# Kernel optimization log

Hardware: AMD Instinct MI355X
Metric: run time of the kernel (lower is better)

## Reference

```python
import jax, jax.numpy as jnp
import numpy as np

H = 8          # n_heads
THRESH = 0.5   # edge pruning threshold
LN_EPS = 1e-5


def setup_inputs() -> dict:
    key = jax.random.key(0)
    ks = jax.random.split(key, 24)
    B, S, D = 8, 128, 256
    N = S + 1
    hd = D // H

    def lin(k, fan_in, fan_out, gain=1.0):
        # xavier_uniform-ish init, stored as [in, out] (y = x @ W + b)
        lim = gain * np.sqrt(6.0 / (fan_in + fan_out))
        return jax.random.uniform(k, (fan_in, fan_out), jnp.float32, -lim, lim)

    g = 1.0 / np.sqrt(2.0)
    return {
        "desc": jax.random.normal(ks[0], (B, S, D), jnp.float32),
        "nv": jax.random.normal(ks[1], (B, N, D), jnp.float32),
        "W_gt": lin(ks[2], D, D), "b_gt": jnp.zeros((D,), jnp.float32),
        "topo_bias": jnp.zeros((1,), jnp.float32),
        "W_q": lin(ks[3], D, D, g), "b_q": jnp.zeros((D,), jnp.float32),
        "W_k": lin(ks[4], D, D, g), "b_k": jnp.zeros((D,), jnp.float32),
        "W_v": lin(ks[5], D, D, g), "b_v": jnp.zeros((D,), jnp.float32),
        "W_e1": lin(ks[6], 2 * D, D), "b_e1": jnp.zeros((D,), jnp.float32),
        "ln_g": jnp.ones((D,), jnp.float32), "ln_b": jnp.zeros((D,), jnp.float32),
        "W_e2": lin(ks[7], D, D), "b_e2": jnp.zeros((D,), jnp.float32),
        "w_attn": lin(ks[8], 3 * hd, 1, g)[:, 0], "b_attn": jnp.zeros((), jnp.float32),
        "W_o": lin(ks[9], D, D, g), "b_o": jnp.zeros((D,), jnp.float32),
    }


def _forward(desc, nv, W_gt, b_gt, topo_bias, W_q, b_q, W_k, b_k, W_v, b_v,
             W_e1, b_e1, ln_g, ln_b, W_e2, b_e2, w_attn, b_attn, W_o, b_o):
    B, N, D = nv.shape
    S = N - 1
    hd = D // H

    # 1. global topology
    d = desc @ W_gt + b_gt                                   # [B,S,D]
    dn = d / jnp.linalg.norm(d, axis=-1, keepdims=True)
    global_top = jax.nn.sigmoid(jnp.einsum('bid,bjd->bij', dn, dn) + topo_bias[0])

    # 2. sample-wise similarity
    var = nv[:, 1:, :]
    vn = var / jnp.linalg.norm(var, axis=-1, keepdims=True)
    sample_sim = jnp.einsum('bid,bjd->bij', vn, vn)
    adj_mat = global_top * sample_sim

    # 3. remove self-connection, squash
    diag_mask = 1.0 - jnp.eye(S, dtype=adj_mat.dtype)
    adj = jax.nn.sigmoid(adj_mat * diag_mask)

    # 4. straight-through edge pruning (frozen=False path)
    hard = (adj > THRESH).astype(adj.dtype)
    adj = hard - jax.lax.stop_gradient(adj) + adj

    # 5. edge attributes: Linear(concat(d_i,d_j)) decomposed into two matmuls
    a = d @ W_e1[:D]                                          # node_i part [B,S,D]
    b_ = d @ W_e1[D:]                                         # node_j part [B,S,D]
    pre = jnp.zeros((B, N, N, D), dtype=d.dtype)
    pre = pre.at[:, 1:, 1:].set(a[:, :, None, :] + b_[:, None, :, :])
    cls = a + b_                                              # concat(d_j,d_j) rows
    pre = pre.at[:, 0, 1:].set(cls).at[:, 1:, 0].set(cls)
    pre = pre + b_e1                                          # (0,0) entry = bias only (zeros input)
    mu = pre.mean(-1, keepdims=True)
    vr = ((pre - mu) ** 2).mean(-1, keepdims=True)
    e = jax.nn.relu((pre - mu) * jax.lax.rsqrt(vr + LN_EPS) * ln_g + ln_b)
    e = e @ W_e2 + b_e2                                       # [B,N,N,D]
    e = e.reshape(B, N, N, H, hd).transpose(0, 3, 1, 2, 4)    # [B,H,N,N,hd]

    # padded adjacency: CLS row attends to all vars, col 0 masked
    na = jnp.zeros((B, N, N), dtype=adj.dtype)
    na = na.at[:, 1:, 1:].set(adj).at[:, 0, 1:].set(1.0)
    e = e * na[:, None, :, :, None]

    # 6. additive attention: attn_proj(concat(q,k,e)) decomposed
    q = (nv @ W_q + b_q).reshape(B, N, H, hd).transpose(0, 2, 1, 3)
    k = (nv @ W_k + b_k).reshape(B, N, H, hd).transpose(0, 2, 1, 3)
    v = (nv @ W_v + b_v).reshape(B, N, H, hd).transpose(0, 2, 1, 3)
    wq, wk, we = w_attn[:hd], w_attn[hd:2 * hd], w_attn[2 * hd:]
    scores = (jnp.einsum('bhid,d->bhi', q, wq)[:, :, :, None]
              + jnp.einsum('bhjd,d->bhj', k, wk)[:, :, None, :]
              + jnp.einsum('bhijd,d->bhij', e, we) + b_attn)
    scores = scores + (na[:, None, :, :] == 0).astype(scores.dtype) * -1e9
    attn = jax.nn.softmax(scores, axis=-1)                    # dropout = identity (eval)

    ctx = jnp.einsum('bhij,bhjd->bhid', attn, v)
    out = ctx.transpose(0, 2, 1, 3).reshape(B, N, D) @ W_o + b_o
    return out, attn


def reference(desc, nv, W_gt, b_gt, topo_bias, W_q, b_q, W_k, b_k, W_v, b_v,
              W_e1, b_e1, ln_g, ln_b, W_e2, b_e2, w_attn, b_attn, W_o, b_o):
    return _forward(desc, nv, W_gt, b_gt, topo_bias, W_q, b_q, W_k, b_k, W_v, b_v,
                    W_e1, b_e1, ln_g, ln_b, W_e2, b_e2, w_attn, b_attn, W_o, b_o)
```

## Files before the change

kernel.cpp:

```cpp
#include <hip/hip_runtime.h>
#include <math.h>

#define BB 8
#define SS 128
#define NN 129
#define DD 256
#define HH 8
#define LN_EPS 1e-5f

#define OFF_A    0
#define OFF_BPT  262144
#define OFF_CPT  524288
#define OFF_VART 786432
#define OFF_V    1048576
#define OFF_SQ   1312768
#define OFF_SK   1321024
#define OFF_MA   1329280
#define OFF_QA   1330304
#define OFF_MB   1331328
#define OFF_QB   1332352
#define OFF_MC   1333376
#define OFF_QC   1334400
#define OFF_U    1335424
#define OFF_UB   1337472

struct SA {
    float dsc[4][DD];
    float drow[4][DD];
    float4 red[8][4][64];
    float part[24][4];
};
struct SB {
    float rows[2][DD];
    float4 redq[8][2][64];
    float4 redk[8][2][64];
};
union SMA { SA a; SB b; };

__global__ __launch_bounds__(512) void ka_all(
    const float* __restrict__ desc, const float* __restrict__ nv,
    const float* __restrict__ W_gt, const float* __restrict__ b_gt,
    const float* __restrict__ W_e1, const float* __restrict__ b_e1,
    const float* __restrict__ W_q, const float* __restrict__ b_q,
    const float* __restrict__ W_k, const float* __restrict__ b_k,
    const float* __restrict__ W_v, const float* __restrict__ b_v,
    const float* __restrict__ W_e2, const float* __restrict__ b_e2,
    const float* __restrict__ w_attn,
    float* __restrict__ a, float* __restrict__ bp_t, float* __restrict__ cp_t,
    float* __restrict__ var_t, float* __restrict__ v,
    float* __restrict__ sq, float* __restrict__ sk,
    float* __restrict__ ma, float* __restrict__ qa, float* __restrict__ mb,
    float* __restrict__ qb, float* __restrict__ mc, float* __restrict__ qc,
    float* __restrict__ U, float* __restrict__ ubias) {
    __shared__ SMA sm;
    const int bx = blockIdx.x, t = threadIdx.x;

    if (bx < 256) {
// ... 102 lines not shown
            for (int r = 0; r < 4; r++) nvv[r] = nv[(size_t)(b * NN + 1 + s0 + r) * DD + d2];
            f4.x = nvv[0]; f4.y = nvv[1]; f4.z = nvv[2]; f4.w = nvv[3];
            *(float4*)(var_t + (size_t)(b * DD + d2) * SS + s0) = f4;
            float vals[24];
#pragma unroll
            for (int r = 0; r < 4; r++) {
                vals[r * 6 + 0] = avf[r]; vals[r * 6 + 1] = avf[r] * avf[r];
                vals[r * 6 + 2] = bvf[r]; vals[r * 6 + 3] = bvf[r] * bvf[r];
                vals[r * 6 + 4] = cvf[r]; vals[r * 6 + 5] = cvf[r] * cvf[r];
            }
            int lane = t & 63, wid = t >> 6;
#pragma unroll
            for (int vv = 0; vv < 24; vv++) {
                float x = vals[vv];
                for (int o = 32; o; o >>= 1) x += __shfl_xor(x, o, 64);
                if (lane == 0) S.part[vv][wid] = x;
            }
        }
        __syncthreads();
        if (t < 24) {
            float ssum = (S.part[t][0] + S.part[t][1]) + (S.part[t][2] + S.part[t][3]);
            int st = t % 6;
            int row = b * SS + s0 + t / 6;
            float m = ssum * (1.f / DD);
            float* dstp = (st == 0) ? ma : (st == 1) ? qa : (st == 2) ? mb
                         : (st == 3) ? qb : (st == 4) ? mc : qc;
            dstp[row] = m;
        }
    } else if (bx < 776) {
        SB& S = sm.b;
        const int idx = bx - 256;
        const int b = idx / 65, n0 = (idx % 65) * 2;
        const int dq = t & 63, kh = t >> 6;
        if (t < 512) {
            int r = t >> 8, d2 = t & 255;
            int n = n0 + r; if (n >= NN) n = NN - 1;
            S.rows[r][d2] = nv[(size_t)(b * NN + n) * DD + d2];
        }
        __syncthreads();
        {
            float4 aq[2], ak[2];
#pragma unroll
            for (int r = 0; r < 2; r++) { aq[r] = make_float4(0.f, 0.f, 0.f, 0.f); ak[r] = aq[r]; }
            const int kb = kh * 32;
#pragma unroll 4
            for (int k = kb; k < kb + 32; k++) {
                float4 wq = *(const float4*)&W_q[k * DD + 4 * dq];
                float4 wk = *(const float4*)&W_k[k * DD + 4 * dq];
#pragma unroll
                for (int r = 0; r < 2; r++) {
                    float x = S.rows[r][k];
                    aq[r].x = fmaf(x, wq.x, aq[r].x); aq[r].y = fmaf(x, wq.y, aq[r].y);
                    aq[r].z = fmaf(x, wq.z, aq[r].z); aq[r].w = fmaf(x, wq.w, aq[r].w);
                    ak[r].x = fmaf(x, wk.x, ak[r].x); ak[r].y = fmaf(x, wk.y, ak[r].y);
                    ak[r].z = fmaf(x, wk.z, ak[r].z); ak[r].w = fmaf(x, wk.w, ak[r].w);
                }
            }
#pragma unroll
            for (int r = 0; r < 2; r++) { S.redq[kh][r][dq] = aq[r]; S.redk[kh][r][dq] = ak[r]; }
        }
        __syncthreads();
        {
            const int d2 = t & 255, r = t >> 8;
            const int n = n0 + r;
            float qf = b_q[d2], kf = b_k[d2];
#pragma unroll
            for (int kk = 0; kk < 8; kk++) {
// ... 32 lines not shown
        {
            const int d2 = t & 255, r = t >> 8;
            const int n = n0 + r;
            if (n < NN) {
                float vf = b_v[d2];
#pragma unroll
                for (int kk = 0; kk < 8; kk++) vf += ((const float*)S.redq[kk][r])[d2];
                v[(size_t)(b * NN + n) * DD + d2] = vf;
            }
        }
    } else {
        const int ri = bx - 776;
        if (t < 256) {
            const int c = t;
            const float wec = w_attn[64 + (c & 31)];
#pragma unroll
            for (int rr = 0; rr < 4; rr++) {
                int r = ri * 4 + rr;
                float x = W_e2[(size_t)r * DD + c] * wec;
#pragma unroll
                for (int o = 16; o; o >>= 1) x += __shfl_xor(x, o, 32);
                if ((c & 31) == 0) U[r * HH + (c >> 5)] = x;
            }
            if (ri == 0) {
                float x = b_e2[c] * wec;
#pragma unroll
                for (int o = 16; o; o >>= 1) x += __shfl_xor(x, o, 32);
                if ((c & 31) == 0) ubias[c >> 5] = x;
            }
        }
    }
}

__global__ __launch_bounds__(256) void kb_scores(
    const float* __restrict__ a, const float* __restrict__ bp_t, const float* __restrict__ cp_t,
    const float* __restrict__ var_t, const float* __restrict__ nv,
    const float* __restrict__ ma, const float* __restrict__ qa,
    const float* __restrict__ mb, const float* __restrict__ qb,
    const float* __restrict__ mc, const float* __restrict__ qc,
    const float* __restrict__ sq, const float* __restrict__ sk,
    const float* __restrict__ ln_g, const float* __restrict__ ln_b,
    const float* __restrict__ U, const float* __restrict__ ubias,
    const float* __restrict__ b_attn,
    float* __restrict__ attn) {
    const int i = blockIdx.x, b = blockIdx.y;
    const int t = threadIdx.x, j = t & 127, dh = t >> 7;
    __shared__ float Arow[DD];
    __shared__ float Vrow[DD];
    __shared__ float2 lnsm[DD];
    __shared__ __attribute__((aligned(16))) float4 Usm[DD][2];
    __shared__ float skm[HH * NN];
    __shared__ float sc[HH][132];
    __shared__ float accred[128][9];
    __shared__ float redc[128][2];
    __shared__ float redv[128][2];

    Arow[t] = (i >= 1) ? a[((size_t)b * SS + i - 1) * DD + t] : 0.f;
    Vrow[t] = nv[((size_t)b * NN + i) * DD + t];
    { float2 g; g.x = ln_g[t]; g.y = ln_b[t]; lnsm[t] = g; }
    Usm[t][0] = *(const float4*)&U[t * HH];
    Usm[t][1] = *(const float4*)&U[t * HH + 4];
    for (int e = t; e < HH * NN; e += 256) skm[e] = sk[(size_t)b * (HH * NN) + e];
    __syncthreads();

    float cr = 0.f, dv = 0.f;
    if (i >= 1) {
        const float* bc = bp_t + ((size_t)b * DD + dh * 128) * SS;
        const float* vc = var_t + ((size_t)b * DD + dh * 128) * SS;
#pragma unroll 8
        for (int dd = 0; dd < 128; dd++) {
            float Bv = bc[(size_t)dd * SS + j];
            float Vv = vc[(size_t)dd * SS + j];
            cr = fmaf(Arow[dh * 128 + dd], Bv, cr);
            dv = fmaf(Vrow[dh * 128 + dd], Vv, dv);
        }
    }
    redc[j][dh] = cr; redv[j][dh] = dv;
    __syncthreads();
    cr = redc[j][0] + redc[j][1];
    dv = redv[j][0] + redv[j][1];
    float rs, nm, mk, pen;
    if (i == 0) {
        float mu = mc[b * SS + j], q2 = qc[b * SS + j];
        rs = rsqrtf(q2 - mu * mu + LN_EPS); nm = -mu * rs; mk = 1.f; pen = 0.f;
    } else {
        float muA = ma[b * SS + i - 1], qA = qa[b * SS + i - 1];
        float muB = mb[b * SS + j],     qB = qb[b * SS + j];
        float mu = muA + muB;
        float var = qA + qB + 2.f * cr * (1.f / DD) - mu * mu;
        rs = rsqrtf(var + LN_EPS); nm = -mu * rs;
        mk = ((i - 1) != j && dv > 0.f) ? 1.f : 0.f;
        pen = (mk == 0.f) ? -1e9f : 0.f;
    }

    float acc[HH];
#pragma unroll
    for (int h = 0; h < HH; h++) acc[h] = 0.f;
    {
        const float* Bp = ((i == 0) ? cp_t : bp_t) + ((size_t)b * DD + dh * 128) * SS;
#pragma unroll 4
        for (int dd = 0; dd < 128; dd++) {
            const int d2 = dh * 128 + dd;
            float Bv = Bp[(size_t)dd * SS + j];
            float pre = Arow[d2] + Bv;
            float y = fmaf(pre, rs, nm);
            float2 gb = lnsm[d2];
            y = fmaf(y, gb.x, gb.y);
            float rr = fmaxf(y, 0.f);
            float4 u0 = Usm[d2][0], u1 = Usm[d2][1];
            acc[0] = fmaf(rr, u0.x, acc[0]); acc[1] = fmaf(rr, u0.y, acc[1]);
            acc[2] = fmaf(rr, u0.z, acc[2]); acc[3] = fmaf(rr, u0.w, acc[3]);
            acc[4] = fmaf(rr, u1.x, acc[4]); acc[5] = fmaf(rr, u1.y, acc[5]);
            acc[6] = fmaf(rr, u1.z, acc[6]); acc[7] = fmaf(rr, u1.w, acc[7]);
        }
    }
    if (dh == 1) {
#pragma unroll
        for (int h = 0; h < HH; h++) accred[j][h] = acc[h];
    }
    __syncthreads();
    if (dh == 0) {
        const float ba = b_attn[0];
#pragma unroll
        for (int h = 0; h < HH; h++) {
            float af = acc[h] + accred[j][h];
            float sqv = sq[(size_t)b * (HH * NN) + h * NN + i];
            sc[h][1 + j] = sqv + skm[h * NN + 1 + j] + (af + ubias[h]) * mk + ba + pen;
        }
        if (j == 0) {
#pragma unroll
            for (int h = 0; h < HH; h++)
                sc[h][0] = sq[(size_t)b * (HH * NN) + h * NN + i] + skm[h * NN] + ba - 1e9f;
        }
    }
    __syncthreads();

    {
        const int h = t >> 5, l = t & 31;
        float m = -INFINITY;
        for (int jj = l; jj < NN; jj += 32) m = fmaxf(m, sc[h][jj]);
#pragma unroll
        for (int o = 16; o; o >>= 1) m = fmaxf(m, __shfl_xor(m, o, 32));
        float s = 0.f;
        for (int jj = l; jj < NN; jj += 32) { float e = __expf(sc[h][jj] - m); sc[h][jj] = e; s += e; }
#pragma unroll
        for (int o = 16; o; o >>= 1) s += __shfl_xor(s, o, 32);
        float inv = 1.f / s;
        float* arow = attn + (((size_t)b * HH + h) * NN + i) * NN;
        for (int jj = l; jj < NN; jj += 32) arow[jj] = sc[h][jj] * inv;
    }
}

__global__ __launch_bounds__(512) void kc_out(
    const float* __restrict__ attn, const float* __restrict__ v,
    const float* __restrict__ W_o, const float* __restrict__ b_o,
    float* __restrict__ out) {
    const int b = blockIdx.y, i0 = blockIdx.x * 4;
    const int t = threadIdx.x;
    __shared__ float ar[4][HH * 133];
    __shared__ float red[2][4][DD];
    __shared__ float csm[4][DD];
    for (int e = t; e < 4 * HH * NN; e += 512) {
        int il = e / (HH * NN), r = e - il * (HH * NN);
        int h = r / NN, jj = r - h * NN;
        int i = i0 + il; if (i > NN - 1) i = NN - 1;
        ar[il][h * 133 + jj] = attn[(((size_t)b * HH + h) * NN + i) * NN + jj];
    }
    __syncthreads();
    {
        const int d = t & 255, jh = t >> 8;
        const int h = d >> 5;
        float cacc[4] = {0.f, 0.f, 0.f, 0.f};
        const int j0 = jh * 65, j1 = (jh == 0) ? 65 : NN;
        for (int jj = j0; jj < j1; jj++) {
            float vv = v[((size_t)b * NN + jj) * DD + d];
            cacc[0] = fmaf(ar[0][h * 133 + jj], vv, cacc[0]);
            cacc[1] = fmaf(ar[1][h * 133 + jj], vv, cacc[1]);
            cacc[2] = fmaf(ar[2][h * 133 + jj], vv, cacc[2]);
            cacc[3] = fmaf(ar[3][h * 133 + jj], vv, cacc[3]);
        }
#pragma unroll
        for (int il = 0; il < 4; il++) red[jh][il][d] = cacc[il];
    }
    __syncthreads();
    for (int e = t; e < 4 * DD; e += 512) {
        int il = e >> 8, d = e & 255;
        csm[il][d] = red[0][il][d] + red[1][il][d];
    }
    __syncthreads();
    {
        const int d2 = t & 255, kh = t >> 8;
        float o[4] = {0.f, 0.f, 0.f, 0.f};
        const int kb = kh * 128;
#pragma unroll 8
        for (int k = kb; k < kb + 128; k++) {
            float w = W_o[(size_t)k * DD + d2];
            o[0] = fmaf(csm[0][k], w, o[0]); o[1] = fmaf(csm[1][k], w, o[1]);
            o[2] = fmaf(csm[2][k], w, o[2]); o[3] = fmaf(csm[3][k], w, o[3]);
        }
#pragma unroll
        for (int il = 0; il < 4; il++) red[kh][il][d2] = o[il];
    }
    __syncthreads();
    for (int e = t; e < 4 * DD; e += 512) {
        int il = e >> 8, d = e & 255;
        int i = i0 + il;
        if (i < NN)
            out[((size_t)b * NN + i) * DD + d] = red[0][il][d] + red[1][il][d] + b_o[d];
    }
}

extern "C" void kernel_launch(void* const* d_in, const int* in_sizes, int n_in,
                              void* d_out, int out_size, void* d_ws, size_t ws_size,
                              hipStream_t stream) {
    const float* desc   = (const float*)d_in[0];
    const float* nv     = (const float*)d_in[1];
    const float* W_gt   = (const float*)d_in[2];
    const float* b_gt   = (const float*)d_in[3];
    const float* W_q    = (const float*)d_in[5];
    const float* b_q    = (const float*)d_in[6];
    const float* W_k    = (const float*)d_in[7];
    const float* b_k    = (const float*)d_in[8];
    const float* W_v    = (const float*)d_in[9];
    const float* b_v    = (const float*)d_in[10];
    const float* W_e1   = (const float*)d_in[11];
    const float* b_e1   = (const float*)d_in[12];
    const float* ln_g   = (const float*)d_in[13];
    const float* ln_b   = (const float*)d_in[14];
    const float* W_e2   = (const float*)d_in[15];
    const float* b_e2   = (const float*)d_in[16];
    const float* w_attn = (const float*)d_in[17];
    const float* b_attn = (const float*)d_in[18];
    const float* W_o    = (const float*)d_in[19];
    const float* b_o    = (const float*)d_in[20];

    float* ws   = (float*)d_ws;
    float* a    = ws + OFF_A;
    float* bp_t = ws + OFF_BPT;
    float* cp_t = ws + OFF_CPT;
    float* vart = ws + OFF_VART;
    float* v    = ws + OFF_V;
    float* sq   = ws + OFF_SQ;
    float* sk   = ws + OFF_SK;
    float* ma   = ws + OFF_MA;
    float* qa   = ws + OFF_QA;
    float* mb   = ws + OFF_MB;
    float* qb   = ws + OFF_QB;
    float* mc   = ws + OFF_MC;
    float* qc   = ws + OFF_QC;
    float* U    = ws + OFF_U;
    float* ub   = ws + OFF_UB;

    float* out  = (float*)d_out;
    float* attn = (float*)d_out + (size_t)BB * NN * DD;

    ka_all<<<dim3(840), dim3(512), 0, stream>>>(
        desc, nv, W_gt, b_gt, W_e1, b_e1, W_q, b_q, W_k, b_k, W_v, b_v,
        W_e2, b_e2, w_attn,
        a, bp_t, cp_t, vart, v, sq, sk, ma, qa, mb, qb, mc, qc, U, ub);
    kb_scores<<<dim3(NN, BB), dim3(256), 0, stream>>>(
        a, bp_t, cp_t, vart, nv, ma, qa, mb, qb, mc, qc, sq, sk,
        ln_g, ln_b, U, ub, b_attn, attn);
    kc_out<<<dim3((NN + 3) / 4, BB), dim3(512), 0, stream>>>(attn, v, W_o, b_o, out);
}
```

Measured before the change: 189.8 us.

## Precompute Gram matrices in separate kernel and process two query rows per block

Moves the per-row dot products (A·B cross term and var·var sign check) out of the scores kernel into a new tiled Gram kernel that computes 16x64 tiles per block with shared A rows. The scores kernel now handles two rows i per block with two j columns per thread, reusing each loaded bp_t value, the LayerNorm parameters and U across four outputs. This cuts redundant global reads of bp_t/var_t but adds a kernel launch and an extra workspace round-trip for G and VV. The scores block count halves, which reduces parallelism.

```diff
diff --git a/kernel.cpp b/kernel.cpp
--- a/kernel.cpp
+++ b/kernel.cpp
@@ -23,6 +23,8 @@
 #define OFF_QC   1334400
 #define OFF_U    1335424
 #define OFF_UB   1337472
+#define OFF_G    1337600
+#define OFF_VV   1468672
 
 struct SA {
     float dsc[4][DD];
@@ -191,7 +193,7 @@
         const int idx = bx - 256;
         const int b = idx / 65, n0 = (idx % 65) * 2;
         const int dq = t & 63, kh = t >> 6;
-        if (t < 512) {
+        {
             int r = t >> 8, d2 = t & 255;
             int n = n0 + r; if (n >= NN) n = NN - 1;
             S.rows[r][d2] = nv[(size_t)(b * NN + n) * DD + d2];
@@ -290,155 +292,254 @@
     }
 }
 
-__global__ __launch_bounds__(256) void kb_scores(
+__global__ __launch_bounds__(256) void kgram(
+    const float* __restrict__ a, const float* __restrict__ bp_t,
+    const float* __restrict__ nv, const float* __restrict__ var_t,
+    float* __restrict__ G, float* __restrict__ VV) {
+    const int bx = blockIdx.x, t = threadIdx.x;
+    const bool isG = bx < 128;
+    const int idx = isG ? bx : bx - 128;
+    const int b = idx >> 4, tl = idx & 15;
+    const int i0 = (tl >> 1) * 16, j0 = (tl & 1) * 64;
+    const float* Asrc = isG ? (a + ((size_t)b * SS + i0) * DD)
+                            : (nv + ((size_t)b * NN + 1 + i0) * DD);
+    const float* Bt = (isG ? bp_t : var_t) + (size_t)b * DD * SS;
+    float* C = (isG ? G : VV) + (size_t)b * SS * SS;
+    __shared__ __attribute__((aligned(16))) float Al[16][DD];
+    for (int e = t; e < 16 * DD / 4; e += 256) {
+        int r = e >> 6, c4 = e & 63;
+        *(float4*)&Al[r][c4 * 4] = *(const float4*)&Asrc[(size_t)r * DD + c4 * 4];
+    }
+    __syncthreads();
+    const int dg = t & 3, jl = t >> 2;
+    float acc[16] = {0.f, 0.f, 0.f, 0.f, 0.f, 0.f, 0.f, 0.f,
+                     0.f, 0.f, 0.f, 0.f, 0.f, 0.f, 0.f, 0.f};
+    const float* bp = Bt + (size_t)(dg * 64) * SS + j0 + jl;
+#pragma unroll 4
+    for (int dd = 0; dd < 64; dd++) {
+        float bvv = bp[(size_t)dd * SS];
+        int d = dg * 64 + dd;
+#pragma unroll
+        for (int i = 0; i < 16; i++) acc[i] = fmaf(Al[i][d], bvv, acc[i]);
+    }
+#pragma unroll
+    for (int i = 0; i < 16; i++) {
+        acc[i] += __shfl_xor(acc[i], 1);
+        acc[i] += __shfl_xor(acc[i], 2);
+    }
+    if (dg == 0) {
+#pragma unroll
+        for (int i = 0; i < 16; i++) C[(size_t)(i0 + i) * SS + j0 + jl] = acc[i];
+    }
+}
+
+__global__ __launch_bounds__(256) void kb4(
     const float* __restrict__ a, const float* __restrict__ bp_t, const float* __restrict__ cp_t,
-    const float* __restrict__ var_t, const float* __restrict__ nv,
     const float* __restrict__ ma, const float* __restrict__ qa,
     const float* __restrict__ mb, const float* __restrict__ qb,
     const float* __restrict__ mc, const float* __restrict__ qc,
+    const float* __restrict__ G, const float* __restrict__ VV,
     const float* __restrict__ sq, const float* __restrict__ sk,
     const float* __restrict__ ln_g, const float* __restrict__ ln_b,
     const float* __restrict__ U, const float* __restrict__ ubias,
     const float* __restrict__ b_attn,
     float* __restrict__ attn) {
-    const int i = blockIdx.x, b = blockIdx.y;
-    const int t = threadIdx.x, j = t & 127, dh = t >> 7;
-    __shared__ float Arow[DD];
-    __shared__ float Vrow[DD];
-    __shared__ float2 lnsm[DD];
+    const int it = blockIdx.x, b = blockIdx.y;
+    const int i0 = it * 2;
+    const int t = threadIdx.x;
+    const int dg = t >> 6, jl = t & 63;
+    __shared__ float Arow[2][DD];
+    __shared__ __attribute__((aligned(8))) float2 lnsm[DD];
     __shared__ __attribute__((aligned(16))) float4 Usm[DD][2];
+    __shared__ __attribute__((aligned(8))) float rsm[2][SS], nmm[2][SS], mkm[2][SS], pnm[2][SS];
     __shared__ float skm[HH * NN];
-    __shared__ float sc[HH][132];
-    __shared__ float accred[128][9];
-    __shared__ float redc[128][2];
-    __shared__ float redv[128][2];
-
-    Arow[t] = (i >= 1) ? a[((size_t)b * SS + i - 1) * DD + t] : 0.f;
-    Vrow[t] = nv[((size_t)b * NN + i) * DD + t];
-    { float2 g; g.x = ln_g[t]; g.y = ln_b[t]; lnsm[t] = g; }
-    Usm[t][0] = *(const float4*)&U[t * HH];
-    Usm[t][1] = *(const float4*)&U[t * HH + 4];
-    for (int e = t; e < HH * NN; e += 256) skm[e] = sk[(size_t)b * (HH * NN) + e];
-    __syncthreads();
-
-    float cr = 0.f, dv = 0.f;
-    if (i >= 1) {
-        const float* bc = bp_t + ((size_t)b * DD + dh * 128) * SS;
-        const float* vc = var_t + ((size_t)b * DD + dh * 128) * SS;
-#pragma unroll 8
-        for (int dd = 0; dd < 128; dd++) {
-            float Bv = bc[(size_t)dd * SS + j];
-            float Vv = vc[(size_t)dd * SS + j];
-            cr = fmaf(Arow[dh * 128 + dd], Bv, cr);
-            dv = fmaf(Vrow[dh * 128 + dd], Vv, dv);
-        }
-    }
-    redc[j][dh] = cr; redv[j][dh] = dv;
-    __syncthreads();
-    cr = redc[j][0] + redc[j][1];
-    dv = redv[j][0] + redv[j][1];
-    float rs, nm, mk, pen;
-    if (i == 0) {
-        float mu = mc[b * SS + j], q2 = qc[b * SS + j];
-        rs = rsqrtf(q2 - mu * mu + LN_EPS); nm = -mu * rs; mk = 1.f; pen = 0.f;
-    } else {
-        float muA = ma[b * SS + i - 1], qA = qa[b * SS + i - 1];
-        float muB = mb[b * SS + j],     qB = qb[b * SS + j];
-        float mu = muA + muB;
-        float var = qA + qB + 2.f * cr * (1.f / DD) - mu * mu;
-        rs = rsqrtf(var + LN_EPS); nm = -mu * rs;
-        mk = ((i - 1) != j && dv > 0.f) ? 1.f : 0.f;
-        pen = (mk == 0.f) ? -1e9f : 0.f;
-    }
-
-    float acc[HH];
-#pragma unroll
-    for (int h = 0; h < HH; h++) acc[h] = 0.f;
+    __shared__ float sqb[2][HH], ubm[HH];
+    __shared__ float sc[2][HH][NN + 3];
+    __shared__ __attribute__((aligned(8))) float red[4][2][HH][SS];
+
     {
-        const float* Bp = ((i == 0) ? cp_t : bp_t) + ((size_t)b * DD + dh * 128) * SS;
-#pragma unroll 4
-        for (int dd = 0; dd < 128; dd++) {
-            const int d2 = dh * 128 + dd;
-            float Bv = Bp[(size_t)dd * SS + j];
-            float pre = Arow[d2] + Bv;
-            float y = fmaf(pre, rs, nm);
-            float2 gb = lnsm[d2];
-            y = fmaf(y, gb.x, gb.y);
-            float rr = fmaxf(y, 0.f);
-            float4 u0 = Usm[d2][0], u1 = Usm[d2][1];
-            acc[0] = fmaf(rr, u0.x, acc[0]); acc[1] = fmaf(rr, u0.y, acc[1]);
-            acc[2] = fmaf(rr, u0.z, acc[2]); acc[3] = fmaf(rr, u0.w, acc[3]);
-            acc[4] = fmaf(rr, u1.x, acc[4]); acc[5] = fmaf(rr, u1.y, acc[5]);
-            acc[6] = fmaf(rr, u1.z, acc[6]); acc[7] = fmaf(rr, u1.w, acc[7]);
-        }
-    }
-    if (dh == 1) {
-#pragma unroll
-        for (int h = 0; h < HH; h++) accred[j][h] = acc[h];
-    }
-    __syncthreads();
-    if (dh == 0) {
-        const float ba = b_attn[0];
+        int ic0 = i0, ic1 = (i0 + 1 < NN) ? i0 + 1 : NN - 1;
+        Arow[0][t] = (ic0 >= 1) ? a[((size_t)b * SS + ic0 - 1) * DD + t] : 0.f;
+        Arow[1][t] = (ic1 >= 1) ? a[((size_t)b * SS + ic1 - 1) * DD + t] : 0.f;
+        float2 g; g.x = ln_g[t]; g.y = ln_b[t]; lnsm[t] = g;
+        Usm[t][0] = *(const float4*)&U[t * HH];
+        Usm[t][1] = *(const float4*)&U[t * HH + 4];
+        for (int e = t; e < HH * NN; e += 256) skm[e] = sk[(size_t)b * HH * NN + e];
+        if (t < 16) {
+            int il = t >> 3, h = t & 7;
+            int i = i0 + il; if (i > NN - 1) i = NN - 1;
+            sqb[il][h] = sq[(size_t)b * HH * NN + h * NN + i] + b_attn[0];
+        }
+        if (t < HH) ubm[t] = ubias[t];
+    }
+    __syncthreads();
+    if (t < SS) {
+        const int j = t;
+#pragma unroll
+        for (int il = 0; il < 2; il++) {
+            int i = i0 + il; if (i > NN - 1) i = NN - 1;
+            float rs, nm, mk, pen;
+            if (i == 0) {
+                float mu = mc[b * SS + j], q2 = qc[b * SS + j];
+                rs = rsqrtf(q2 - mu * mu + LN_EPS); nm = -mu * rs; mk = 1.f; pen = 0.f;
+            } else {
+                float cr = G[((size_t)b * SS + i - 1) * SS + j];
+                float dv = VV[((size_t)b * SS + i - 1) * SS + j];
+                float muA = ma[b * SS + i - 1], qA = qa[b * SS + i - 1];
+                float muB = mb[b * SS + j], qB = qb[b * SS + j];
+                float mu = muA + muB;
+                float var = qA + qB + 2.f * cr * (1.f / DD) - mu * mu;
+                rs = rsqrtf(var + LN_EPS); nm = -mu * rs;
+                mk = ((i - 1) != j && dv > 0.f) ? 1.f : 0.f;
+                pen = (mk == 0.f) ? -1e9f : 0.f;
+            }
+            rsm[il][j] = rs; nmm[il][j] = nm; mkm[il][j] = mk; pnm[il][j] = pen;
+        }
+    }
+    __syncthreads();
+    float acc[2][HH][2];
+#pragma unroll
+    for (int il = 0; il < 2; il++)
+#pragma unroll
+        for (int h = 0; h < HH; h++) { acc[il][h][0] = 0.f; acc[il][h][1] = 0.f; }
+    {
+        const float* Bb = bp_t + ((size_t)b * DD + dg * 64) * SS + 2 * jl;
+        float2 r0 = *(const float2*)&rsm[0][2 * jl];
+        float2 n0 = *(const float2*)&nmm[0][2 * jl];
+        float2 r1 = *(const float2*)&rsm[1][2 * jl];
+        float2 n1 = *(const float2*)&nmm[1][2 * jl];
+        if (i0 != 0) {
+#pragma unroll 4
+            for (int dd = 0; dd < 64; dd++) {
+                const int d = dg * 64 + dd;
+                float2 bv = *(const float2*)(Bb + (size_t)dd * SS);
+                float A0 = Arow[0][d], A1 = Arow[1][d];
+                float2 gb = lnsm[d];
+                float4 u0 = Usm[d][0], u1 = Usm[d][1];
+                float y0 = fmaf(A0 + bv.x, r0.x, n0.x); y0 = fmaf(y0, gb.x, gb.y);
+                float y1 = fmaf(A0 + bv.y, r0.y, n0.y); y1 = fmaf(y1, gb.x, gb.y);
+                float e0 = fmaxf(y0, 0.f), e1 = fmaxf(y1, 0.f);
+                float z0 = fmaf(A1 + bv.x, r1.x, n1.x); z0 = fmaf(z0, gb.x, gb.y);
+                float z1 = fmaf(A1 + bv.y, r1.y, n1.y); z1 = fmaf(z1, gb.x, gb.y);
+                float f0 = fmaxf(z0, 0.f), f1 = fmaxf(z1, 0.f);
+                acc[0][0][0] = fmaf(e0, u0.x, acc[0][0][0]); acc[0][0][1] = fmaf(e1, u0.x, acc[0][0][1]);
+                acc[0][1][0] = fmaf(e0, u0.y, acc[0][1][0]); acc[0][1][1] = fmaf(e1, u0.y, acc[0][1][1]);
+                acc[0][2][0] = fmaf(e0, u0.z, acc[0][2][0]); acc[0][2][1] = fmaf(e1, u0.z, acc[0][2][1]);
+                acc[0][3][0] = fmaf(e0, u0.w, acc[0][3][0]); acc[0][3][1] = fmaf(e1, u0.w, acc[0][3][1]);
+                acc[0][4][0] = fmaf(e0, u1.x, acc[0][4][0]); acc[0][4][1] = fmaf(e1, u1.x, acc[0][4][1]);
+                acc[0][5][0] = fmaf(e0, u1.y, acc[0][5][0]); acc[0][5][1] = fmaf(e1, u1.y, acc[0][5][1]);
+                acc[0][6][0] = fmaf(e0, u1.z, acc[0][6][0]); acc[0][6][1] = fmaf(e1, u1.z, acc[0][6][1]);
+                acc[0][7][0] = fmaf(e0, u1.w, acc[0][7][0]); acc[0][7][1] = fmaf(e1, u1.w, acc[0][7][1]);
+                acc[1][0][0] = fmaf(f0, u0.x, acc[1][0][0]); acc[1][0][1] = fmaf(f1, u0.x, acc[1][0][1]);
+                acc[1][1][0] = fmaf(f0, u0.y, acc[1][1][0]); acc[1][1][1] = fmaf(f1, u0.y, acc[1][1][1]);
+                acc[1][2][0] = fmaf(f0, u0.z, acc[1][2][0]); acc[1][2][1] = fmaf(f1, u0.z, acc[1][2][1]);
+                acc[1][3][0] = fmaf(f0, u0.w, acc[1][3][0]); acc[1][3][1] = fmaf(f1, u0.w, acc[1][3][1]);
+                acc[1][4][0] = fmaf(f0, u1.x, acc[1][4][0]); acc[1][4][1] = fmaf(f1, u1.x, acc[1][4][1]);
+                acc[1][5][0] = fmaf(f0, u1.y, acc[1][5][0]); acc[1][5][1] = fmaf(f1, u1.y, acc[1][5][1]);
+                acc[1][6][0] = fmaf(f0, u1.z, acc[1][6][0]); acc[1][6][1] = fmaf(f1, u1.z, acc[1][6][1]);
+                acc[1][7][0] = fmaf(f0, u1.w, acc[1][7][0]); acc[1][7][1] = fmaf(f1, u1.w, acc[1][7][1]);
+            }
+        } else {
+            const float* Bc = cp_t + ((size_t)b * DD + dg * 64) * SS + 2 * jl;
+#pragma unroll 4
+            for (int dd = 0; dd < 64; dd++) {
+                const int d = dg * 64 + dd;
+                float2 bA = *(const float2*)(Bc + (size_t)dd * SS);
+                float2 bB = *(const float2*)(Bb + (size_t)dd * SS);
+                float A0 = Arow[0][d], A1 = Arow[1][d];
+                float2 gb = lnsm[d];
+                float4 u0 = Usm[d][0], u1 = Usm[d][1];
+                float y0 = fmaf(A0 + bA.x, r0.x, n0.x); y0 = fmaf(y0, gb.x, gb.y);
+                float y1 = fmaf(A0 + bA.y, r0.y, n0.y); y1 = fmaf(y1, gb.x, gb.y);
+                float e0 = fmaxf(y0, 0.f), e1 = fmaxf(y1, 0.f);
+                float z0 = fmaf(A1 + bB.x, r1.x, n1.x); z0 = fmaf(z0, gb.x, gb.y);
+                float z1 = fmaf(A1 + bB.y, r1.y, n1.y); z1 = fmaf(z1, gb.x, gb.y);
+                float f0 = fmaxf(z0, 0.f), f1 = fmaxf(z1, 0.f);
+                acc[0][0][0] = fmaf(e0, u0.x, acc[0][0][0]); acc[0][0][1] = fmaf(e1, u0.x, acc[0][0][1]);
+                acc[0][1][0] = fmaf(e0, u0.y, acc[0][1][0]); acc[0][1][1] = fmaf(e1, u0.y, acc[0][1][1]);
+                acc[0][2][0] = fmaf(e0, u0.z, acc[0][2][0]); acc[0][2][1] = fmaf(e1, u0.z, acc[0][2][1]);
+                acc[0][3][0] = fmaf(e0, u0.w, acc[0][3][0]); acc[0][3][1] = fmaf(e1, u0.w, acc[0][3][1]);
+                acc[0][4][0] = fmaf(e0, u1.x, acc[0][4][0]); acc[0][4][1] = fmaf(e1, u1.x, acc[0][4][1]);
+                acc[0][5][0] = fmaf(e0, u1.y, acc[0][5][0]); acc[0][5][1] = fmaf(e1, u1.y, acc[0][5][1]);
+                acc[0][6][0] = fmaf(e0, u1.z, acc[0][6][0]); acc[0][6][1] = fmaf(e1, u1.z, acc[0][6][1]);
+                acc[0][7][0] = fmaf(e0, u1.w, acc[0][7][0]); acc[0][7][1] = fmaf(e1, u1.w, acc[0][7][1]);
+                acc[1][0][0] = fmaf(f0, u0.x, acc[1][0][0]); acc[1][0][1] = fmaf(f1, u0.x, acc[1][0][1]);
+                acc[1][1][0] = fmaf(f0, u0.y, acc[1][1][0]); acc[1][1][1] = fmaf(f1, u0.y, acc[1][1][1]);
+                acc[1][2][0] = fmaf(f0, u0.z, acc[1][2][0]); acc[1][2][1] = fmaf(f1, u0.z, acc[1][2][1]);
+                acc[1][3][0] = fmaf(f0, u0.w, acc[1][3][0]); acc[1][3][1] = fmaf(f1, u0.w, acc[1][3][1]);
+                acc[1][4][0] = fmaf(f0, u1.x, acc[1][4][0]); acc[1][4][1] = fmaf(f1, u1.x, acc[1][4][1]);
+                acc[1][5][0] = fmaf(f0, u1.y, acc[1][5][0]); acc[1][5][1] = fmaf(f1, u1.y, acc[1][5][1]);
+                acc[1][6][0] = fmaf(f0, u1.z, acc[1][6][0]); acc[1][6][1] = fmaf(f1, u1.z, acc[1][6][1]);
+                acc[1][7][0] = fmaf(f0, u1.w, acc[1][7][0]); acc[1][7][1] = fmaf(f1, u1.w, acc[1][7][1]);
+            }
+        }
+    }
+#pragma unroll
+    for (int il = 0; il < 2; il++)
 #pragma unroll
         for (int h = 0; h < HH; h++) {
-            float af = acc[h] + accred[j][h];
-            float sqv = sq[(size_t)b * (HH * NN) + h * NN + i];
-            sc[h][1 + j] = sqv + skm[h * NN + 1 + j] + (af + ubias[h]) * mk + ba + pen;
-        }
-        if (j == 0) {
-#pragma unroll
-            for (int h = 0; h < HH; h++)
-                sc[h][0] = sq[(size_t)b * (HH * NN) + h * NN + i] + skm[h * NN] + ba - 1e9f;
-        }
-    }
-    __syncthreads();
-
+            float2 w; w.x = acc[il][h][0]; w.y = acc[il][h][1];
+            *(float2*)&red[dg][il][h][2 * jl] = w;
+        }
+    __syncthreads();
+    for (int e = t; e < 2 * HH * SS; e += 256) {
+        int il = e >> 10, h = (e >> 7) & 7, j = e & 127;
+        float s = (red[0][il][h][j] + red[1][il][h][j]) + (red[2][il][h][j] + red[3][il][h][j]);
+        sc[il][h][1 + j] = sqb[il][h] + skm[h * NN + 1 + j] + (s + ubm[h]) * mkm[il][j] + pnm[il][j];
+    }
+    if (t < 16) { int il = t >> 3, h = t & 7; sc[il][h][0] = sqb[il][h] + skm[h * NN] - 1e9f; }
+    __syncthreads();
     {
-        const int h = t >> 5, l = t & 31;
+        const int row = t >> 4, l = t & 15;
+        const int il = row >> 3, h = row & 7;
+        const int i = i0 + il;
         float m = -INFINITY;
-        for (int jj = l; jj < NN; jj += 32) m = fmaxf(m, sc[h][jj]);
-#pragma unroll
-        for (int o = 16; o; o >>= 1) m = fmaxf(m, __shfl_xor(m, o, 32));
+        for (int j = l; j < NN; j += 16) m = fmaxf(m, sc[il][h][j]);
+#pragma unroll
+        for (int o = 8; o; o >>= 1) m = fmaxf(m, __shfl_xor(m, o, 16));
         float s = 0.f;
-        for (int jj = l; jj < NN; jj += 32) { float e = __expf(sc[h][jj] - m); sc[h][jj] = e; s += e; }
-#pragma unroll
-        for (int o = 16; o; o >>= 1) s += __shfl_xor(s, o, 32);
+        for (int j = l; j < NN; j += 16) { float e = __expf(sc[il][h][j] - m); sc[il][h][j] = e; s += e; }
+#pragma unroll
+        for (int o = 8; o; o >>= 1) s += __shfl_xor(s, o, 16);
         float inv = 1.f / s;
-        float* arow = attn + (((size_t)b * HH + h) * NN + i) * NN;
-        for (int jj = l; jj < NN; jj += 32) arow[jj] = sc[h][jj] * inv;
+        if (i < NN) {
+            float* arow = attn + (((size_t)b * HH + h) * NN + i) * NN;
+            for (int j = l; j < NN; j += 16) arow[j] = sc[il][h][j] * inv;
+        }
     }
 }
 
-__global__ __launch_bounds__(512) void kc_out(
+__global__ __launch_bounds__(512) void kc4(
     const float* __restrict__ attn, const float* __restrict__ v,
     const float* __restrict__ W_o, const float* __restrict__ b_o,
     float* __restrict__ out) {
     const int b = blockIdx.y, i0 = blockIdx.x * 4;
     const int t = threadIdx.x;
-    __shared__ float ar[4][HH * 133];
+    __shared__ float ar[4][HH * 132];
     __shared__ float red[2][4][DD];
     __shared__ float csm[4][DD];
     for (int e = t; e < 4 * HH * NN; e += 512) {
-        int il = e / (HH * NN), r = e - il * (HH * NN);
-        int h = r / NN, jj = r - h * NN;
-        int i = i0 + il; if (i > NN - 1) i = NN - 1;
-        ar[il][h * 133 + jj] = attn[(((size_t)b * HH + h) * NN + i) * NN + jj];
+        int il = e / (HH * NN), rem = e - il * (HH * NN);
+        int h = rem / NN, j = rem - h * NN;
+        int i = i0 + il; if (i >= NN) i = NN - 1;
+        ar[il][h * 132 + j] = attn[(((size_t)b * HH + h) * NN + i) * NN + j];
     }
     __syncthreads();
     {
         const int d = t & 255, jh = t >> 8;
         const int h = d >> 5;
-        float cacc[4] = {0.f, 0.f, 0.f, 0.f};
-        const int j0 = jh * 65, j1 = (jh == 0) ? 65 : NN;
-        for (int jj = j0; jj < j1; jj++) {
-            float vv = v[((size_t)b * NN + jj) * DD + d];
-            cacc[0] = fmaf(ar[0][h * 133 + jj], vv, cacc[0]);
-            cacc[1] = fmaf(ar[1][h * 133 + jj], vv, cacc[1]);
-            cacc[2] = fmaf(ar[2][h * 133 + jj], vv, cacc[2]);
-            cacc[3] = fmaf(ar[3][h * 133 + jj], vv, cacc[3]);
-        }
-#pragma unroll
-        for (int il = 0; il < 4; il++) red[jh][il][d] = cacc[il];
+        float c0 = 0.f, c1 = 0.f, c2 = 0.f, c3 = 0.f;
+        const float* vp = v + (size_t)b * NN * DD + d;
+        const int j0 = jh * 65, j1 = jh ? NN : 65;
+#pragma unroll 4
+        for (int j = j0; j < j1; j++) {
+            float vv = vp[(size_t)j * DD];
+            c0 = fmaf(ar[0][h * 132 + j], vv, c0);
+            c1 = fmaf(ar[1][h * 132 + j], vv, c1);
+            c2 = fmaf(ar[2][h * 132 + j], vv, c2);
+            c3 = fmaf(ar[3][h * 132 + j], vv, c3);
+        }
+        red[jh][0][d] = c0; red[jh][1][d] = c1; red[jh][2][d] = c2; red[jh][3][d] = c3;
     }
     __syncthreads();
     for (int e = t; e < 4 * DD; e += 512) {
@@ -447,17 +548,16 @@
     }
     __syncthreads();
     {
-        const int d2 = t & 255, kh = t >> 8;
-        float o[4] = {0.f, 0.f, 0.f, 0.f};
+        const int c = t & 255, kh = t >> 8;
+        float o0 = 0.f, o1 = 0.f, o2 = 0.f, o3 = 0.f;
         const int kb = kh * 128;
 #pragma unroll 8
         for (int k = kb; k < kb + 128; k++) {
-            float w = W_o[(size_t)k * DD + d2];
-            o[0] = fmaf(csm[0][k], w, o[0]); o[1] = fmaf(csm[1][k], w, o[1]);
-            o[2] = fmaf(csm[2][k], w, o[2]); o[3] = fmaf(csm[3][k], w, o[3]);
-        }
-#pragma unroll
-        for (int il = 0; il < 4; il++) red[kh][il][d2] = o[il];
+            float w = W_o[(size_t)k * DD + c];
+            o0 = fmaf(csm[0][k], w, o0); o1 = fmaf(csm[1][k], w, o1);
+            o2 = fmaf(csm[2][k], w, o2); o3 = fmaf(csm[3][k], w, o3);
+        }
+        red[kh][0][c] = o0; red[kh][1][c] = o1; red[kh][2][c] = o2; red[kh][3][c] = o3;
     }
     __syncthreads();
     for (int e = t; e < 4 * DD; e += 512) {
@@ -508,6 +608,8 @@
     float* qc   = ws + OFF_QC;
     float* U    = ws + OFF_U;
     float* ub   = ws + OFF_UB;
+    float* G    = ws + OFF_G;
+    float* VV   = ws + OFF_VV;
 
     float* out  = (float*)d_out;
     float* attn = (float*)d_out + (size_t)BB * NN * DD;
@@ -516,8 +618,9 @@
         desc, nv, W_gt, b_gt, W_e1, b_e1, W_q, b_q, W_k, b_k, W_v, b_v,
         W_e2, b_e2, w_attn,
         a, bp_t, cp_t, vart, v, sq, sk, ma, qa, mb, qb, mc, qc, U, ub);
-    kb_scores<<<dim3(NN, BB), dim3(256), 0, stream>>>(
-        a, bp_t, cp_t, vart, nv, ma, qa, mb, qb, mc, qc, sq, sk,
+    kgram<<<dim3(256), dim3(256), 0, stream>>>(a, bp_t, nv, vart, G, VV);
+    kb4<<<dim3(65, BB), dim3(256), 0, stream>>>(
+        a, bp_t, cp_t, ma, qa, mb, qb, mc, qc, G, VV, sq, sk,
         ln_g, ln_b, U, ub, b_attn, attn);
-    kc_out<<<dim3((NN + 3) / 4, BB), dim3(512), 0, stream>>>(attn, v, W_o, b_o, out);
+    kc4<<<dim3(33, BB), dim3(512), 0, stream>>>(attn, v, W_o, b_o, out);
 }
```

Result: faster. 185.3 us (-2.4%).

## Fuse score, softmax, attn@V and output projection into one kernel

Applied to the files above, without the earlier changes.

Merges the score/softmax kernel with the context and output-projection kernel, so each (i,b) block keeps its softmax row in shared memory and computes ctx and out directly. This removes one launch and the re-read of attn from global memory. The score loop is also remapped so each thread handles two j columns over a 64-wide d slice, using float2 loads and wave shuffles instead of shared-memory reductions. The cost is that W_o is now read once per row (per block) instead of once per four rows, and V is re-read by every row block.

```diff
diff --git a/kernel.cpp b/kernel.cpp
--- a/kernel.cpp
+++ b/kernel.cpp
@@ -191,7 +191,7 @@
         const int idx = bx - 256;
         const int b = idx / 65, n0 = (idx % 65) * 2;
         const int dq = t & 63, kh = t >> 6;
-        if (t < 512) {
+        {
             int r = t >> 8, d2 = t & 255;
             int n = n0 + r; if (n >= NN) n = NN - 1;
             S.rows[r][d2] = nv[(size_t)(b * NN + n) * DD + d2];
@@ -290,9 +290,10 @@
     }
 }
 
-__global__ __launch_bounds__(256) void kb_scores(
+__global__ __launch_bounds__(256) void kmega4(
     const float* __restrict__ a, const float* __restrict__ bp_t, const float* __restrict__ cp_t,
     const float* __restrict__ var_t, const float* __restrict__ nv,
+    const float* __restrict__ v,
     const float* __restrict__ ma, const float* __restrict__ qa,
     const float* __restrict__ mb, const float* __restrict__ qb,
     const float* __restrict__ mc, const float* __restrict__ qc,
@@ -300,171 +301,196 @@
     const float* __restrict__ ln_g, const float* __restrict__ ln_b,
     const float* __restrict__ U, const float* __restrict__ ubias,
     const float* __restrict__ b_attn,
-    float* __restrict__ attn) {
+    const float* __restrict__ W_o, const float* __restrict__ b_o,
+    float* __restrict__ attn, float* __restrict__ out) {
     const int i = blockIdx.x, b = blockIdx.y;
-    const int t = threadIdx.x, j = t & 127, dh = t >> 7;
+    const int t = threadIdx.x;
+    const int w = t >> 6, l = t & 63;
+    const int dgp = l >> 4;
+    const int jp = w * 16 + (l & 15);
+
     __shared__ float Arow[DD];
-    __shared__ float Vrow[DD];
-    __shared__ float2 lnsm[DD];
+    __shared__ __attribute__((aligned(8))) float2 lnsm[DD];
     __shared__ __attribute__((aligned(16))) float4 Usm[DD][2];
+    __shared__ __attribute__((aligned(8))) float rsm[SS], nmm[SS], mkm[SS], pnm[SS];
     __shared__ float skm[HH * NN];
-    __shared__ float sc[HH][132];
-    __shared__ float accred[128][9];
-    __shared__ float redc[128][2];
-    __shared__ float redv[128][2];
-
-    Arow[t] = (i >= 1) ? a[((size_t)b * SS + i - 1) * DD + t] : 0.f;
-    Vrow[t] = nv[((size_t)b * NN + i) * DD + t];
-    { float2 g; g.x = ln_g[t]; g.y = ln_b[t]; lnsm[t] = g; }
-    Usm[t][0] = *(const float4*)&U[t * HH];
-    Usm[t][1] = *(const float4*)&U[t * HH + 4];
-    for (int e = t; e < HH * NN; e += 256) skm[e] = sk[(size_t)b * (HH * NN) + e];
-    __syncthreads();
-
-    float cr = 0.f, dv = 0.f;
+    __shared__ float sqb[HH], ubm[HH];
+    __shared__ float sc[HH][NN + 3];
+    __shared__ union { float Vrow[DD]; float csm[DD]; } uv;
+    __shared__ __attribute__((aligned(16))) union {
+        struct { float crs[SS]; float dvs[SS]; } p1;
+        float redc[4][DD];
+    } ur;
+
+    {
+        Arow[t] = (i >= 1) ? a[((size_t)b * SS + i - 1) * DD + t] : 0.f;
+        uv.Vrow[t] = nv[((size_t)b * NN + i) * DD + t];
+        float2 g; g.x = ln_g[t]; g.y = ln_b[t]; lnsm[t] = g;
+        Usm[t][0] = *(const float4*)&U[t * HH];
+        Usm[t][1] = *(const float4*)&U[t * HH + 4];
+        for (int e = t; e < HH * NN; e += 256) skm[e] = sk[(size_t)b * HH * NN + e];
+        if (t < HH) {
+            sqb[t] = sq[(size_t)b * HH * NN + t * NN + i] + b_attn[0];
+            ubm[t] = ubias[t];
+        }
+    }
+    __syncthreads();
+
     if (i >= 1) {
-        const float* bc = bp_t + ((size_t)b * DD + dh * 128) * SS;
-        const float* vc = var_t + ((size_t)b * DD + dh * 128) * SS;
+        float cr[2] = {0.f, 0.f}, dvv[2] = {0.f, 0.f};
+        const float* bc = bp_t + ((size_t)b * DD + dgp * 64) * SS + 2 * jp;
+        const float* vc = var_t + ((size_t)b * DD + dgp * 64) * SS + 2 * jp;
 #pragma unroll 8
-        for (int dd = 0; dd < 128; dd++) {
-            float Bv = bc[(size_t)dd * SS + j];
-            float Vv = vc[(size_t)dd * SS + j];
-            cr = fmaf(Arow[dh * 128 + dd], Bv, cr);
-            dv = fmaf(Vrow[dh * 128 + dd], Vv, dv);
-        }
-    }
-    redc[j][dh] = cr; redv[j][dh] = dv;
-    __syncthreads();
-    cr = redc[j][0] + redc[j][1];
-    dv = redv[j][0] + redv[j][1];
-    float rs, nm, mk, pen;
-    if (i == 0) {
-        float mu = mc[b * SS + j], q2 = qc[b * SS + j];
-        rs = rsqrtf(q2 - mu * mu + LN_EPS); nm = -mu * rs; mk = 1.f; pen = 0.f;
-    } else {
-        float muA = ma[b * SS + i - 1], qA = qa[b * SS + i - 1];
-        float muB = mb[b * SS + j],     qB = qb[b * SS + j];
-        float mu = muA + muB;
-        float var = qA + qB + 2.f * cr * (1.f / DD) - mu * mu;
-        rs = rsqrtf(var + LN_EPS); nm = -mu * rs;
-        mk = ((i - 1) != j && dv > 0.f) ? 1.f : 0.f;
-        pen = (mk == 0.f) ? -1e9f : 0.f;
-    }
-
-    float acc[HH];
-#pragma unroll
-    for (int h = 0; h < HH; h++) acc[h] = 0.f;
+        for (int dd = 0; dd < 64; dd++) {
+            float2 bv = *(const float2*)(bc + (size_t)dd * SS);
+            float2 vv = *(const float2*)(vc + (size_t)dd * SS);
+            const int d = dgp * 64 + dd;
+            float A0 = Arow[d], V0 = uv.Vrow[d];
+            cr[0] = fmaf(A0, bv.x, cr[0]); cr[1] = fmaf(A0, bv.y, cr[1]);
+            dvv[0] = fmaf(V0, vv.x, dvv[0]); dvv[1] = fmaf(V0, vv.y, dvv[1]);
+        }
+#pragma unroll
+        for (int jj = 0; jj < 2; jj++) {
+            float c = cr[jj], d2 = dvv[jj];
+            c += __shfl_xor(c, 16); c += __shfl_xor(c, 32);
+            d2 += __shfl_xor(d2, 16); d2 += __shfl_xor(d2, 32);
+            cr[jj] = c; dvv[jj] = d2;
+        }
+        if (l < 16) {
+            float2 wc; wc.x = cr[0]; wc.y = cr[1];
+            float2 wd; wd.x = dvv[0]; wd.y = dvv[1];
+            *(float2*)&ur.p1.crs[2 * jp] = wc;
+            *(float2*)&ur.p1.dvs[2 * jp] = wd;
+        }
+    }
+    __syncthreads();
+    if (t < SS) {
+        const int j = t;
+        float rs, nm, mk, pen;
+        if (i == 0) {
+            float mu = mc[b * SS + j], q2 = qc[b * SS + j];
+            rs = rsqrtf(q2 - mu * mu + LN_EPS); nm = -mu * rs; mk = 1.f; pen = 0.f;
+        } else {
+            float cr = ur.p1.crs[j];
+            float dv = ur.p1.dvs[j];
+            float muA = ma[b * SS + i - 1], qA = qa[b * SS + i - 1];
+            float muB = mb[b * SS + j], qB = qb[b * SS + j];
+            float mu = muA + muB;
+            float var = qA + qB + 2.f * cr * (1.f / DD) - mu * mu;
+            rs = rsqrtf(var + LN_EPS); nm = -mu * rs;
+            mk = ((i - 1) != j && dv > 0.f) ? 1.f : 0.f;
+            pen = (mk == 0.f) ? -1e9f : 0.f;
+        }
+        rsm[j] = rs; nmm[j] = nm; mkm[j] = mk; pnm[j] = pen;
+    }
+    __syncthreads();
+    float acc[HH][2];
+#pragma unroll
+    for (int h = 0; h < HH; h++) { acc[h][0] = 0.f; acc[h][1] = 0.f; }
     {
-        const float* Bp = ((i == 0) ? cp_t : bp_t) + ((size_t)b * DD + dh * 128) * SS;
-#pragma unroll 4
-        for (int dd = 0; dd < 128; dd++) {
-            const int d2 = dh * 128 + dd;
-            float Bv = Bp[(size_t)dd * SS + j];
-            float pre = Arow[d2] + Bv;
-            float y = fmaf(pre, rs, nm);
-            float2 gb = lnsm[d2];
-            y = fmaf(y, gb.x, gb.y);
-            float rr = fmaxf(y, 0.f);
-            float4 u0 = Usm[d2][0], u1 = Usm[d2][1];
-            acc[0] = fmaf(rr, u0.x, acc[0]); acc[1] = fmaf(rr, u0.y, acc[1]);
-            acc[2] = fmaf(rr, u0.z, acc[2]); acc[3] = fmaf(rr, u0.w, acc[3]);
-            acc[4] = fmaf(rr, u1.x, acc[4]); acc[5] = fmaf(rr, u1.y, acc[5]);
-            acc[6] = fmaf(rr, u1.z, acc[6]); acc[7] = fmaf(rr, u1.w, acc[7]);
-        }
-    }
-    if (dh == 1) {
-#pragma unroll
-        for (int h = 0; h < HH; h++) accred[j][h] = acc[h];
-    }
-    __syncthreads();
-    if (dh == 0) {
-        const float ba = b_attn[0];
+        const float* Bp = ((i == 0) ? cp_t : bp_t) + ((size_t)b * DD + dgp * 64) * SS + 2 * jp;
+        float2 r0 = *(const float2*)&rsm[2 * jp];
+        float2 n0 = *(const float2*)&nmm[2 * jp];
+#pragma unroll 8
+        for (int dd = 0; dd < 64; dd++) {
+            const int d = dgp * 64 + dd;
+            float2 bv = *(const float2*)(Bp + (size_t)dd * SS);
+            float A0 = Arow[d];
+            float2 gb = lnsm[d];
+            float4 u0 = Usm[d][0], u1 = Usm[d][1];
+            float y0 = fmaf(A0 + bv.x, r0.x, n0.x); y0 = fmaf(y0, gb.x, gb.y);
+            float y1 = fmaf(A0 + bv.y, r0.y, n0.y); y1 = fmaf(y1, gb.x, gb.y);
+            float e0 = fmaxf(y0, 0.f), e1 = fmaxf(y1, 0.f);
+            acc[0][0] = fmaf(e0, u0.x, acc[0][0]); acc[0][1] = fmaf(e1, u0.x, acc[0][1]);
+            acc[1][0] = fmaf(e0, u0.y, acc[1][0]); acc[1][1] = fmaf(e1, u0.y, acc[1][1]);
+            acc[2][0] = fmaf(e0, u0.z, acc[2][0]); acc[2][1] = fmaf(e1, u0.z, acc[2][1]);
+            acc[3][0] = fmaf(e0, u0.w, acc[3][0]); acc[3][1] = fmaf(e1, u0.w, acc[3][1]);
+            acc[4][0] = fmaf(e0, u1.x, acc[4][0]); acc[4][1] = fmaf(e1, u1.x, acc[4][1]);
+            acc[5][0] = fmaf(e0, u1.y, acc[5][0]); acc[5][1] = fmaf(e1, u1.y, acc[5][1]);
+            acc[6][0] = fmaf(e0, u1.z, acc[6][0]); acc[6][1] = fmaf(e1, u1.z, acc[6][1]);
+            acc[7][0] = fmaf(e0, u1.w, acc[7][0]); acc[7][1] = fmaf(e1, u1.w, acc[7][1]);
+        }
+    }
+#pragma unroll
+    for (int h = 0; h < HH; h++) {
+        float s0 = acc[h][0], s1 = acc[h][1];
+        s0 += __shfl_xor(s0, 16); s0 += __shfl_xor(s0, 32);
+        s1 += __shfl_xor(s1, 16); s1 += __shfl_xor(s1, 32);
+        acc[h][0] = s0; acc[h][1] = s1;
+    }
+    if (l < 16) {
+        const int j0 = 2 * jp, j1 = j0 + 1;
+        float mk0 = mkm[j0], pn0 = pnm[j0];
+        float mk1 = mkm[j1], pn1 = pnm[j1];
 #pragma unroll
         for (int h = 0; h < HH; h++) {
-            float af = acc[h] + accred[j][h];
-            float sqv = sq[(size_t)b * (HH * NN) + h * NN + i];
-            sc[h][1 + j] = sqv + skm[h * NN + 1 + j] + (af + ubias[h]) * mk + ba + pen;
-        }
-        if (j == 0) {
-#pragma unroll
-            for (int h = 0; h < HH; h++)
-                sc[h][0] = sq[(size_t)b * (HH * NN) + h * NN + i] + skm[h * NN] + ba - 1e9f;
-        }
-    }
-    __syncthreads();
-
+            sc[h][1 + j0] = sqb[h] + skm[h * NN + 1 + j0] + (acc[h][0] + ubm[h]) * mk0 + pn0;
+            sc[h][1 + j1] = sqb[h] + skm[h * NN + 1 + j1] + (acc[h][1] + ubm[h]) * mk1 + pn1;
+        }
+    }
+    if (t < HH) sc[t][0] = sqb[t] + skm[t * NN] - 1e9f;
+    __syncthreads();
     {
-        const int h = t >> 5, l = t & 31;
+        const int h = t >> 5, ll = t & 31;
         float m = -INFINITY;
-        for (int jj = l; jj < NN; jj += 32) m = fmaxf(m, sc[h][jj]);
+        for (int j = ll; j < NN; j += 32) m = fmaxf(m, sc[h][j]);
 #pragma unroll
         for (int o = 16; o; o >>= 1) m = fmaxf(m, __shfl_xor(m, o, 32));
         float s = 0.f;
-        for (int jj = l; jj < NN; jj += 32) { float e = __expf(sc[h][jj] - m); sc[h][jj] = e; s += e; }
+        float ev[5];
+        int cnt = 0;
+        for (int j = ll; j < NN; j += 32) { float e = __expf(sc[h][j] - m); ev[cnt++] = e; s += e; }
 #pragma unroll
         for (int o = 16; o; o >>= 1) s += __shfl_xor(s, o, 32);
         float inv = 1.f / s;
         float* arow = attn + (((size_t)b * HH + h) * NN + i) * NN;
-        for (int jj = l; jj < NN; jj += 32) arow[jj] = sc[h][jj] * inv;
-    }
-}
-
-__global__ __launch_bounds__(512) void kc_out(
-    const float* __restrict__ attn, const float* __restrict__ v,
-    const float* __restrict__ W_o, const float* __restrict__ b_o,
-    float* __restrict__ out) {
-    const int b = blockIdx.y, i0 = blockIdx.x * 4;
-    const int t = threadIdx.x;
-    __shared__ float ar[4][HH * 133];
-    __shared__ float red[2][4][DD];
-    __shared__ float csm[4][DD];
-    for (int e = t; e < 4 * HH * NN; e += 512) {
-        int il = e / (HH * NN), r = e - il * (HH * NN);
-        int h = r / NN, jj = r - h * NN;
-        int i = i0 + il; if (i > NN - 1) i = NN - 1;
-        ar[il][h * 133 + jj] = attn[(((size_t)b * HH + h) * NN + i) * NN + jj];
+        cnt = 0;
+        for (int j = ll; j < NN; j += 32) {
+            float p = ev[cnt++] * inv;
+            sc[h][j] = p;
+            arow[j] = p;
+        }
     }
     __syncthreads();
     {
-        const int d = t & 255, jh = t >> 8;
-        const int h = d >> 5;
-        float cacc[4] = {0.f, 0.f, 0.f, 0.f};
-        const int j0 = jh * 65, j1 = (jh == 0) ? 65 : NN;
-        for (int jj = j0; jj < j1; jj++) {
-            float vv = v[((size_t)b * NN + jj) * DD + d];
-            cacc[0] = fmaf(ar[0][h * 133 + jj], vv, cacc[0]);
-            cacc[1] = fmaf(ar[1][h * 133 + jj], vv, cacc[1]);
-            cacc[2] = fmaf(ar[2][h * 133 + jj], vv, cacc[2]);
-            cacc[3] = fmaf(ar[3][h * 133 + jj], vv, cacc[3]);
-        }
-#pragma unroll
-        for (int il = 0; il < 4; il++) red[jh][il][d] = cacc[il];
-    }
-    __syncthreads();
-    for (int e = t; e < 4 * DD; e += 512) {
-        int il = e >> 8, d = e & 255;
-        csm[il][d] = red[0][il][d] + red[1][il][d];
-    }
+        const int dq = t & 63, jg = t >> 6;
+        const int h = dq >> 3;
+        float ca[4] = {0.f, 0.f, 0.f, 0.f};
+#pragma unroll 8
+        for (int jj = 0; jj < 33; jj++) {
+            int j = jg * 33 + jj;
+            if (j < NN) {
+                float4 vv = *(const float4*)&v[((size_t)b * NN + j) * DD + 4 * dq];
+                float p0 = sc[h][j];
+                ca[0] = fmaf(p0, vv.x, ca[0]); ca[1] = fmaf(p0, vv.y, ca[1]);
+                ca[2] = fmaf(p0, vv.z, ca[2]); ca[3] = fmaf(p0, vv.w, ca[3]);
+            }
+        }
+        float4 wv; wv.x = ca[0]; wv.y = ca[1]; wv.z = ca[2]; wv.w = ca[3];
+        *(float4*)&ur.redc[jg][4 * dq] = wv;
+    }
+    __syncthreads();
+    uv.csm[t] = (ur.redc[0][t] + ur.redc[1][t]) + (ur.redc[2][t] + ur.redc[3][t]);
     __syncthreads();
     {
-        const int d2 = t & 255, kh = t >> 8;
+        const int cq = t & 63, kg = t >> 6;
         float o[4] = {0.f, 0.f, 0.f, 0.f};
-        const int kb = kh * 128;
 #pragma unroll 8
-        for (int k = kb; k < kb + 128; k++) {
-            float w = W_o[(size_t)k * DD + d2];
-            o[0] = fmaf(csm[0][k], w, o[0]); o[1] = fmaf(csm[1][k], w, o[1]);
-            o[2] = fmaf(csm[2][k], w, o[2]); o[3] = fmaf(csm[3][k], w, o[3]);
-        }
-#pragma unroll
-        for (int il = 0; il < 4; il++) red[kh][il][d2] = o[il];
-    }
-    __syncthreads();
-    for (int e = t; e < 4 * DD; e += 512) {
-        int il = e >> 8, d = e & 255;
-        int i = i0 + il;
-        if (i < NN)
-            out[((size_t)b * NN + i) * DD + d] = red[0][il][d] + red[1][il][d] + b_o[d];
+        for (int kk = 0; kk < 64; kk++) {
+            int k = kg * 64 + kk;
+            float4 wv = *(const float4*)&W_o[(size_t)k * DD + 4 * cq];
+            float c0 = uv.csm[k];
+            o[0] = fmaf(c0, wv.x, o[0]); o[1] = fmaf(c0, wv.y, o[1]);
+            o[2] = fmaf(c0, wv.z, o[2]); o[3] = fmaf(c0, wv.w, o[3]);
+        }
+        __syncthreads();
+        float4 wv; wv.x = o[0]; wv.y = o[1]; wv.z = o[2]; wv.w = o[3];
+        *(float4*)&ur.redc[kg][4 * cq] = wv;
+    }
+    __syncthreads();
+    {
+        float s = (ur.redc[0][t] + ur.redc[1][t]) + (ur.redc[2][t] + ur.redc[3][t]) + b_o[t];
+        out[((size_t)b * NN + i) * DD + t] = s;
     }
 }
 
@@ -516,8 +542,7 @@
         desc, nv, W_gt, b_gt, W_e1, b_e1, W_q, b_q, W_k, b_k, W_v, b_v,
         W_e2, b_e2, w_attn,
         a, bp_t, cp_t, vart, v, sq, sk, ma, qa, mb, qb, mc, qc, U, ub);
-    kb_scores<<<dim3(NN, BB), dim3(256), 0, stream>>>(
-        a, bp_t, cp_t, vart, nv, ma, qa, mb, qb, mc, qc, sq, sk,
-        ln_g, ln_b, U, ub, b_attn, attn);
-    kc_out<<<dim3((NN + 3) / 4, BB), dim3(512), 0, stream>>>(attn, v, W_o, b_o, out);
+    kmega4<<<dim3(NN, BB), dim3(256), 0, stream>>>(
+        a, bp_t, cp_t, vart, nv, v, ma, qa, mb, qb, mc, qc, sq, sk,
+        ln_g, ln_b, U, ub, b_attn, W_o, b_o, attn, out);
 }
```

After: 178.2 us. -6.1%, faster.
